# Kernel optimization log

Measured on AMD Instinct MI355X. Metric: run time of the kernel, lower is better.

The kernel has to match this reference:

```python
import jax, jax.numpy as jnp
import numpy as np

N, E, DIM, H = 100000, 1600000, 128, 8
HD = DIM // H


def setup_inputs() -> dict:
    key = jax.random.key(0)
    ks = jax.random.split(key, 12)
    inp = {
        'x': jax.random.normal(ks[0], (N, DIM), dtype=jnp.float32),
        'src': jax.random.randint(ks[1], (E,), 0, N, dtype=jnp.int32),
        'dst': jax.random.randint(ks[2], (E,), 0, N, dtype=jnp.int32),
    }
    scale = 1.0 / np.sqrt(DIM)
    for i, nm in enumerate(['q', 'k', 'v', 'o']):
        inp['W' + nm] = jax.random.normal(ks[3 + 2 * i], (DIM, DIM), dtype=jnp.float32) * scale
        inp['b' + nm] = jax.random.normal(ks[4 + 2 * i], (DIM,), dtype=jnp.float32) * 0.01
    return inp


def reference(x, src, dst, Wq, bq, Wk, bk, Wv, bv, Wo, bo):
    n = x.shape[0]
    q = (x @ Wq + bq).reshape(n, H, HD)
    k = (x @ Wk + bk).reshape(n, H, HD)
    v = (x @ Wv + bv).reshape(n, H, HD)
    # per-edge score: dot(q[src], k[dst]) over head_dim  -> [E, H]
    scores = jnp.einsum('ehd,ehd->eh', q[src], k[dst]) / np.sqrt(HD).astype(np.float32)
    # edge softmax grouped by destination node
    m = jax.ops.segment_max(scores, dst, num_segments=n)        # [N, H]
    e = jnp.exp(scores - m[dst])                                 # [E, H]
    z = jax.ops.segment_sum(e, dst, num_segments=n)              # [N, H]
    attn = e / z[dst]                                            # [E, H]
    # weighted scatter-sum of source values into destinations
    agg = jax.ops.segment_sum(v[src] * attn[:, :, None], dst, num_segments=n)  # [N, H, HD]
    out = agg.reshape(n, DIM) @ Wo + bo
    return out
```

## Files before the change

### kernel.cpp

```cpp
#include <hip/hip_runtime.h>
#include <hip/hip_bf16.h>
#include <math.h>


#define CAP 64
#define BCHUNK 4096

typedef __attribute__((ext_vector_type(8))) short short8;
typedef __attribute__((ext_vector_type(4))) float f32x4;

__device__ inline unsigned short f2bf(float f) {
    unsigned u = __float_as_uint(f);
    unsigned r = u + 0x7fffu + ((u >> 16) & 1u);
    return (unsigned short)(r >> 16);
}
__device__ inline float bfhi2f(unsigned u) { return __uint_as_float(u & 0xffff0000u); }
__device__ inline float bflo2f(unsigned u) { return __uint_as_float(u << 16); }

__device__ inline float w_perm(const float* Wq, const float* Wk, const float* Wv,
                               int k, int c) {
    if (c < 256) {
        int hh = c >> 4, r = c & 15;
        return (r < 8) ? Wq[k * 128 + hh * 8 + r] : Wv[k * 128 + hh * 8 + (r - 8)];
    }
    return Wk[k * 128 + (c - 256)];
}

__global__ void pack_b_kernel(const float* __restrict__ Wq, const float* __restrict__ Wk,
                              const float* __restrict__ Wv, const float* __restrict__ Wo,
                              const float* __restrict__ bq, const float* __restrict__ bk,
                              const float* __restrict__ bv,
                              short* __restrict__ BqkvP, short* __restrict__ BoP,
                              float* __restrict__ bqkv) {
    int t = blockIdx.x * 256 + threadIdx.x;
    if (t < 24 * 4 * 64 * 8) {
        int j = t & 7, l = (t >> 3) & 63, ks = (t >> 9) & 3, ct = t >> 11;
        int c = ct * 16 + (l & 15);
        int k = ks * 32 + (l >> 4) * 8 + j;
        BqkvP[t] = (short)f2bf(w_perm(Wq, Wk, Wv, k, c));
    }
    if (t < 8 * 4 * 64 * 8) {
        int j = t & 7, l = (t >> 3) & 63, ks = (t >> 9) & 3, ct = t >> 11;
        int c = ct * 16 + (l & 15);
        int k = ks * 32 + (l >> 4) * 8 + j;
        BoP[t] = (short)f2bf(Wo[k * 128 + c]);
    }
    if (t < 384) {
        float v;
        if (t < 256) {
            int hh = t >> 4, r = t & 15;
            v = (r < 8) ? bq[hh * 8 + r] : bv[hh * 8 + (r - 8)];
        } else v = bk[t - 256];
        bqkv[t] = v;
    }
}

#define QKV_STRIDE 392
__global__ __launch_bounds__(256) void gemm_qkv_mfma(const float* __restrict__ A,
        const short* __restrict__ Bp, const float* __restrict__ bias,
        short* __restrict__ qv, short* __restrict__ kb, int M) {
    __shared__ short stage[4][16][QKV_STRIDE];
    int w = threadIdx.x >> 6, l = threadIdx.x & 63;
    int row0 = blockIdx.x * 64 + w * 16;
    int lr = l & 15, lk = l >> 4;

    f32x4 acc[24];
    #pragma unroll
    for (int ct = 0; ct < 24; ++ct) {
        float b = bias[ct * 16 + lr];
        acc[ct][0] = b; acc[ct][1] = b; acc[ct][2] = b; acc[ct][3] = b;
    }

    int arow = row0 + lr;
    bool rowok = arow < M;
    const float* arp = A + (size_t)arow * 128;

    #pragma unroll
    for (int ks = 0; ks < 4; ++ks) {
        f32x4 a0 = {0.f, 0.f, 0.f, 0.f}, a1 = {0.f, 0.f, 0.f, 0.f};
        if (rowok) {
            a0 = *(const f32x4*)(arp + ks * 32 + lk * 8);
            a1 = *(const f32x4*)(arp + ks * 32 + lk * 8 + 4);
        }
        short8 af;
        af[0] = (short)f2bf(a0[0]); af[1] = (short)f2bf(a0[1]);
        af[2] = (short)f2bf(a0[2]); af[3] = (short)f2bf(a0[3]);
        af[4] = (short)f2bf(a1[0]); af[5] = (short)f2bf(a1[1]);
        af[6] = (short)f2bf(a1[2]); af[7] = (short)f2bf(a1[3]);
        #pragma unroll
        for (int ct = 0; ct < 24; ++ct) {
            short8 bf = *(const short8*)(Bp + ((size_t)(ct * 4 + ks) * 64 + l) * 8);
            acc[ct] = __builtin_amdgcn_mfma_f32_16x16x32_bf16(af, bf, acc[ct], 0, 0, 0);
        }
    }

    #pragma unroll
    for (int ct = 0; ct < 24; ++ct) {
        int c = ct * 16 + lr;
        #pragma unroll
        for (int j = 0; j < 4; ++j)
            stage[w][lk * 4 + j][c] = (short)f2bf(acc[ct][j]);
    }
    __syncthreads();

    #pragma unroll
    for (int it = 0; it < 8; ++it) {
        int rr = it * 2 + (l >> 5);
        int row = row0 + rr;
        if (row < M) {
            short8 vqv = *(const short8*)&stage[w][rr][(l & 31) * 8];
            *(short8*)(qv + (size_t)row * 256 + (l & 31) * 8) = vqv;
        }
    }
    #pragma unroll
    for (int it = 0; it < 4; ++it) {
        int rr = it * 4 + (l >> 4);
        int row = row0 + rr;
        if (row < M) {
            short8 vk = *(const short8*)&stage[w][rr][256 + (l & 15) * 8];
            *(short8*)(kb + (size_t)row * 128 + (l & 15) * 8) = vk;
        }
    }
}

__global__ __launch_bounds__(256) void build_kernel(const int* __restrict__ src,
        const int* __restrict__ dst, int* __restrict__ cursor, int* __restrict__ csr,
        int E, int per8) {
    int xcd = blockIdx.x & 7;
    int chunk = blockIdx.x >> 3;
    int lo = xcd * per8, hi = lo + per8;
    int base = chunk * BCHUNK;
    #pragma unroll
    for (int it = 0; it < BCHUNK / 256; ++it) {
        int e = base + it * 256 + threadIdx.x;
        if (e < E) {
            int d = dst[e];
            if (d >= lo && d < hi) {
                int s = src[e];
                int slot = atomicAdd(&cursor[d], 1);
                if (slot < CAP) csr[((size_t)d << 6) + slot] = s;
            }
        }
    }
}

#define AGG_STRIDE 68

#define EDGE_ITER(EI, ACT)                                                     \
    {                                                                          \
        bool act = (ACT);                                                      \
        int s = act ? (EI) : 0;                                                \
        const uint4* qp = (const uint4*)(qv + (size_t)s * 256 + h2 * 16);      \
        uint4 qq = qp[0];                                                      \
        uint4 vv = qp[1];                                                      \
        float p = bflo2f(qq.x) * kf[0] + bfhi2f(qq.x) * kf[1]                  \
                + bflo2f(qq.y) * kf[2] + bfhi2f(qq.y) * kf[3]                  \
                + bflo2f(qq.z) * kf[4] + bfhi2f(qq.z) * kf[5]                  \
                + bflo2f(qq.w) * kf[6] + bfhi2f(qq.w) * kf[7];                 \
        p += __shfl_xor(p, 1);                                                 \
        float ee = act ? __expf(p * 0.25f) : 0.f;                              \
        z += ee;                                                               \
        ag[0] += ee * bflo2f(vv.x); ag[1] += ee * bfhi2f(vv.x);                \
        ag[2] += ee * bflo2f(vv.y); ag[3] += ee * bfhi2f(vv.y);                \
        ag[4] += ee * bflo2f(vv.z); ag[5] += ee * bfhi2f(vv.z);                \
        ag[6] += ee * bflo2f(vv.w); ag[7] += ee * bfhi2f(vv.w);                \
    }

__global__ __launch_bounds__(256) void edge_out_kernel(const short* __restrict__ qv,
        const short* __restrict__ kb, const int* __restrict__ cursor,
        const int* __restrict__ csr, const short* __restrict__ BoP,
        const float* __restrict__ bo, float* __restrict__ out, int N, int per8) {
    __shared__ unsigned aggLds[16][AGG_STRIDE];
    int w  = threadIdx.x >> 6;
    int l  = threadIdx.x & 63;
    int lr = l & 15, lk = l >> 4;
    int h2 = l & 15;
    int slot = l >> 4;
    int xcd = blockIdx.x & 7;
    int jb  = blockIdx.x >> 3;
    int sliceN = per8 < (N - xcd * per8) ? per8 : (N - xcd * per8);
    int local0 = jb * 16;

    #pragma unroll
    for (int q = 0; q < 4; ++q) {
        int i = w * 4 + q;
        int local = local0 + i;
        if (local < sliceN) {
            int d = xcd * per8 + local;
            int deg = cursor[d];
            int n = (deg < CAP) ? deg : CAP;
            const int* ep = csr + ((size_t)d << 6);

            uint4 kk = *(const uint4*)(kb + (size_t)d * 128 + h2 * 8);
            float kf[8];
            kf[0] = bflo2f(kk.x); kf[1] = bfhi2f(kk.x);
            kf[2] = bflo2f(kk.y); kf[3] = bfhi2f(kk.y);
            kf[4] = bflo2f(kk.z); kf[5] = bfhi2f(kk.z);
            kf[6] = bflo2f(kk.w); kf[7] = bfhi2f(kk.w);

            float z = 0.f;
            float ag[8] = {0.f, 0.f, 0.f, 0.f, 0.f, 0.f, 0.f, 0.f};

            for (int b0 = 0; b0 < n; b0 += 16) {
                int bb = b0 + slot * 4;
                int4 e4 = *(const int4*)(ep + bb);
                EDGE_ITER(e4.x, bb + 0 < n)
                EDGE_ITER(e4.y, bb + 1 < n)
                EDGE_ITER(e4.z, bb + 2 < n)
                EDGE_ITER(e4.w, bb + 3 < n)
            }

            z += __shfl_xor(z, 16);
            z += __shfl_xor(z, 32);
            #pragma unroll
            for (int j = 0; j < 8; ++j) {
                ag[j] += __shfl_xor(ag[j], 16);
                ag[j] += __shfl_xor(ag[j], 32);
            }

            float zi = (z > 0.f) ? 1.0f / z : 0.f;
            if (slot == 0) {
                #pragma unroll
                for (int j = 0; j < 4; ++j) {
                    unsigned pk = (unsigned)f2bf(ag[2 * j] * zi) |
                                  ((unsigned)f2bf(ag[2 * j + 1] * zi) << 16);
                    aggLds[i][h2 * 4 + j] = pk;
                }
            }
        }
    }
    __syncthreads();

    f32x4 acc[2];
    #pragma unroll
    for (int t = 0; t < 2; ++t) {
        float b = bo[(w * 2 + t) * 16 + lr];
        acc[t][0] = b; acc[t][1] = b; acc[t][2] = b; acc[t][3] = b;
    }

    #pragma unroll
    for (int ks = 0; ks < 4; ++ks) {
        short8 af = *(const short8*)&aggLds[lr][ks * 16 + lk * 4];
        #pragma unroll
        for (int t = 0; t < 2; ++t) {
            int ct = w * 2 + t;
            short8 bf = *(const short8*)(BoP + ((size_t)(ct * 4 + ks) * 64 + l) * 8);
            acc[t] = __builtin_amdgcn_mfma_f32_16x16x32_bf16(af, bf, acc[t], 0, 0, 0);
        }
    }

    #pragma unroll
    for (int t = 0; t < 2; ++t) {
        int c = (w * 2 + t) * 16 + lr;
        #pragma unroll
        for (int j = 0; j < 4; ++j) {
            int localr = local0 + lk * 4 + j;
            if (localr < sliceN) {
                int r = xcd * per8 + localr;
                out[(size_t)r * 128 + c] = acc[t][j];
            }
        }
    }
}

extern "C" void kernel_launch(void* const* d_in, const int* in_sizes, int n_in,
                              void* d_out, int out_size, void* d_ws, size_t ws_size,
                              hipStream_t stream) {
    const float* x   = (const float*)d_in[0];
    const int*   src = (const int*)d_in[1];
    const int*   dst = (const int*)d_in[2];
    const float* Wq  = (const float*)d_in[3];
    const float* bq  = (const float*)d_in[4];
    const float* Wk  = (const float*)d_in[5];
    const float* bk  = (const float*)d_in[6];
    const float* Wv  = (const float*)d_in[7];
    const float* bv  = (const float*)d_in[8];
    const float* Wo  = (const float*)d_in[9];
    const float* bo  = (const float*)d_in[10];
    float* out = (float*)d_out;

    int N = in_sizes[0] / 128;
    int E = in_sizes[1];
    int per8 = (N + 7) / 8;

    char* ws = (char*)d_ws;
    size_t off = 0;
    auto alloc = [&](size_t bytes) -> void* {
        void* p = ws + off;
        off = (off + bytes + 255) & ~(size_t)255;
        return p;
    };
    short* BqkvP  = (short*)alloc((size_t)24 * 4 * 64 * 8 * 2);
    short* BoP    = (short*)alloc((size_t)8 * 4 * 64 * 8 * 2);
    float* bqkv   = (float*)alloc(384 * 4);
    short* qv     = (short*)alloc((size_t)N * 256 * 2);
    short* kb     = (short*)alloc((size_t)N * 128 * 2);
    int* csr      = (int*)alloc((size_t)N * CAP * 4);
    int* cursor   = (int*)alloc((size_t)N * 4);
    (void)ws_size; (void)n_in; (void)out_size;

    hipMemsetAsync(cursor, 0, (size_t)N * 4, stream);

    pack_b_kernel<<<192, 256, 0, stream>>>(Wq, Wk, Wv, Wo, bq, bk, bv, BqkvP, BoP, bqkv);

    gemm_qkv_mfma<<<(N + 63) / 64, 256, 0, stream>>>(x, BqkvP, bqkv, qv, kb, N);

    int nchunks = (E + BCHUNK - 1) / BCHUNK;
    build_kernel<<<nchunks * 8, 256, 0, stream>>>(src, dst, cursor, csr, E, per8);

    int nb16 = (per8 + 15) / 16;
    edge_out_kernel<<<nb16 * 8, 256, 0, stream>>>(qv, kb, cursor, csr, BoP, bo, out, N, per8);
}
```

Measured before the change: 276.6 us.

## Assign one lane per head in edge aggregation and store q/v unpermuted

The packed QKV layout changes from interleaved q/v per half-head to contiguous q (cols 0-127) and v (cols 128-255). The edge kernel now gives each lane a full 16-dim head instead of splitting a head across two lanes. This drops the per-edge shuffle for the dot product and handles 8 edges per wavefront step instead of 4, with four wide loads per edge. In exchange it doubles register state per lane (16 k values and 16 accumulators), adds one more cross-lane reduction stage, and reads edges as scalar ints instead of int4.

```diff
diff --git a/kernel.cpp b/kernel.cpp
--- a/kernel.cpp
+++ b/kernel.cpp
@@ -19,10 +19,8 @@
 
 __device__ inline float w_perm(const float* Wq, const float* Wk, const float* Wv,
                                int k, int c) {
-    if (c < 256) {
-        int hh = c >> 4, r = c & 15;
-        return (r < 8) ? Wq[k * 128 + hh * 8 + r] : Wv[k * 128 + hh * 8 + (r - 8)];
-    }
+    if (c < 128)  return Wq[k * 128 + c];
+    if (c < 256)  return Wv[k * 128 + (c - 128)];
     return Wk[k * 128 + (c - 256)];
 }
 
@@ -47,10 +45,9 @@
     }
     if (t < 384) {
         float v;
-        if (t < 256) {
-            int hh = t >> 4, r = t & 15;
-            v = (r < 8) ? bq[hh * 8 + r] : bv[hh * 8 + (r - 8)];
-        } else v = bk[t - 256];
+        if (t < 128)      v = bq[t];
+        else if (t < 256) v = bv[t - 128];
+        else              v = bk[t - 256];
         bqkv[t] = v;
     }
 }
@@ -150,20 +147,27 @@
     {                                                                          \
         bool act = (ACT);                                                      \
         int s = act ? (EI) : 0;                                                \
-        const uint4* qp = (const uint4*)(qv + (size_t)s * 256 + h2 * 16);      \
-        uint4 qq = qp[0];                                                      \
-        uint4 vv = qp[1];                                                      \
-        float p = bflo2f(qq.x) * kf[0] + bfhi2f(qq.x) * kf[1]                  \
-                + bflo2f(qq.y) * kf[2] + bfhi2f(qq.y) * kf[3]                  \
-                + bflo2f(qq.z) * kf[4] + bfhi2f(qq.z) * kf[5]                  \
-                + bflo2f(qq.w) * kf[6] + bfhi2f(qq.w) * kf[7];                 \
-        p += __shfl_xor(p, 1);                                                 \
+        const uint4* qp = (const uint4*)(qv + (size_t)s * 256 + head * 16);    \
+        uint4 qa = qp[0], qb = qp[1];                                          \
+        uint4 va = qp[16], vb = qp[17];  \
+        float p = bflo2f(qa.x) * kf[0]  + bfhi2f(qa.x) * kf[1]                 \
+                + bflo2f(qa.y) * kf[2]  + bfhi2f(qa.y) * kf[3]                 \
+                + bflo2f(qa.z) * kf[4]  + bfhi2f(qa.z) * kf[5]                 \
+                + bflo2f(qa.w) * kf[6]  + bfhi2f(qa.w) * kf[7]                 \
+                + bflo2f(qb.x) * kf[8]  + bfhi2f(qb.x) * kf[9]                 \
+                + bflo2f(qb.y) * kf[10] + bfhi2f(qb.y) * kf[11]                \
+                + bflo2f(qb.z) * kf[12] + bfhi2f(qb.z) * kf[13]                \
+                + bflo2f(qb.w) * kf[14] + bfhi2f(qb.w) * kf[15];               \
         float ee = act ? __expf(p * 0.25f) : 0.f;                              \
         z += ee;                                                               \
-        ag[0] += ee * bflo2f(vv.x); ag[1] += ee * bfhi2f(vv.x);                \
-        ag[2] += ee * bflo2f(vv.y); ag[3] += ee * bfhi2f(vv.y);                \
-        ag[4] += ee * bflo2f(vv.z); ag[5] += ee * bfhi2f(vv.z);                \
-        ag[6] += ee * bflo2f(vv.w); ag[7] += ee * bfhi2f(vv.w);                \
+        ag[0]  += ee * bflo2f(va.x); ag[1]  += ee * bfhi2f(va.x);              \
+        ag[2]  += ee * bflo2f(va.y); ag[3]  += ee * bfhi2f(va.y);              \
+        ag[4]  += ee * bflo2f(va.z); ag[5]  += ee * bfhi2f(va.z);              \
+        ag[6]  += ee * bflo2f(va.w); ag[7]  += ee * bfhi2f(va.w);              \
+        ag[8]  += ee * bflo2f(vb.x); ag[9]  += ee * bfhi2f(vb.x);              \
+        ag[10] += ee * bflo2f(vb.y); ag[11] += ee * bfhi2f(vb.y);              \
+        ag[12] += ee * bflo2f(vb.z); ag[13] += ee * bfhi2f(vb.z);              \
+        ag[14] += ee * bflo2f(vb.w); ag[15] += ee * bfhi2f(vb.w);              \
     }
 
 __global__ __launch_bounds__(256) void edge_out_kernel(const short* __restrict__ qv,
@@ -174,8 +178,8 @@
     int w  = threadIdx.x >> 6;
     int l  = threadIdx.x & 63;
     int lr = l & 15, lk = l >> 4;
-    int h2 = l & 15;
-    int slot = l >> 4;
+    int head = l & 7;
+    int slot = l >> 3;
     int xcd = blockIdx.x & 7;
     int jb  = blockIdx.x >> 3;
     int sliceN = per8 < (N - xcd * per8) ? per8 : (N - xcd * per8);
@@ -191,29 +195,38 @@
             int n = (deg < CAP) ? deg : CAP;
             const int* ep = csr + ((size_t)d << 6);
 
-            uint4 kk = *(const uint4*)(kb + (size_t)d * 128 + h2 * 8);
-            float kf[8];
-            kf[0] = bflo2f(kk.x); kf[1] = bfhi2f(kk.x);
-            kf[2] = bflo2f(kk.y); kf[3] = bfhi2f(kk.y);
-            kf[4] = bflo2f(kk.z); kf[5] = bfhi2f(kk.z);
-            kf[6] = bflo2f(kk.w); kf[7] = bfhi2f(kk.w);
+            const uint4* kp = (const uint4*)(kb + (size_t)d * 128 + head * 16);
+            uint4 ka = kp[0], kc = kp[1];
+            float kf[16];
+            kf[0]  = bflo2f(ka.x); kf[1]  = bfhi2f(ka.x);
+            kf[2]  = bflo2f(ka.y); kf[3]  = bfhi2f(ka.y);
+            kf[4]  = bflo2f(ka.z); kf[5]  = bfhi2f(ka.z);
+            kf[6]  = bflo2f(ka.w); kf[7]  = bfhi2f(ka.w);
+            kf[8]  = bflo2f(kc.x); kf[9]  = bfhi2f(kc.x);
+            kf[10] = bflo2f(kc.y); kf[11] = bfhi2f(kc.y);
+            kf[12] = bflo2f(kc.z); kf[13] = bfhi2f(kc.z);
+            kf[14] = bflo2f(kc.w); kf[15] = bfhi2f(kc.w);
 
             float z = 0.f;
-            float ag[8] = {0.f, 0.f, 0.f, 0.f, 0.f, 0.f, 0.f, 0.f};
+            float ag[16];
+            #pragma unroll
+            for (int j = 0; j < 16; ++j) ag[j] = 0.f;
 
             for (int b0 = 0; b0 < n; b0 += 16) {
-                int bb = b0 + slot * 4;
-                int4 e4 = *(const int4*)(ep + bb);
-                EDGE_ITER(e4.x, bb + 0 < n)
-                EDGE_ITER(e4.y, bb + 1 < n)
-                EDGE_ITER(e4.z, bb + 2 < n)
-                EDGE_ITER(e4.w, bb + 3 < n)
-            }
-
+                int i0 = b0 + slot;
+                int i1 = b0 + 8 + slot;
+                int eA = ep[i0];
+                int eB = ep[i1];
+                EDGE_ITER(eA, i0 < n)
+                EDGE_ITER(eB, i1 < n)
+            }
+
+            z += __shfl_xor(z, 8);
             z += __shfl_xor(z, 16);
             z += __shfl_xor(z, 32);
             #pragma unroll
-            for (int j = 0; j < 8; ++j) {
+            for (int j = 0; j < 16; ++j) {
+                ag[j] += __shfl_xor(ag[j], 8);
                 ag[j] += __shfl_xor(ag[j], 16);
                 ag[j] += __shfl_xor(ag[j], 32);
             }
@@ -221,10 +234,10 @@
             float zi = (z > 0.f) ? 1.0f / z : 0.f;
             if (slot == 0) {
                 #pragma unroll
-                for (int j = 0; j < 4; ++j) {
+                for (int j = 0; j < 8; ++j) {
                     unsigned pk = (unsigned)f2bf(ag[2 * j] * zi) |
                                   ((unsigned)f2bf(ag[2 * j + 1] * zi) << 16);
-                    aggLds[i][h2 * 4 + j] = pk;
+                    aggLds[i][head * 8 + j] = pk;
                 }
             }
         }
```

After: 276.1 us. Within noise of the previous version (-0.2%).
